# Optimization experiments

Measured on AMD Instinct MI355X. Metric: run time of the kernel, lower is better.

Reference implementation:

```python
import jax, jax.numpy as jnp
import numpy as np

NUM_HEADS = 16


def setup_inputs() -> dict:
    key = jax.random.key(0)
    ks = jax.random.split(key, 10)
    B, C, T, K, E = 2, 4, 512, 1024, 1024
    s = 0.02
    return {
        "hidden_states": jax.random.normal(ks[0], (B, T, E), jnp.float32),
        "key_value_states": jax.random.normal(ks[1], (B, C, K, E), jnp.float32),
        "Wq": jax.random.normal(ks[2], (E, E), jnp.float32) * s,
        "bq": jax.random.normal(ks[3], (E,), jnp.float32) * s,
        "Wk": jax.random.normal(ks[4], (E, E), jnp.float32) * s,
        "bk": jax.random.normal(ks[5], (E,), jnp.float32) * s,
        "Wv": jax.random.normal(ks[6], (E, E), jnp.float32) * s,
        "bv": jax.random.normal(ks[7], (E,), jnp.float32) * s,
        "Wo": jax.random.normal(ks[8], (E, E), jnp.float32) * s,
        "bo": jax.random.normal(ks[9], (E,), jnp.float32) * s,
    }


def reference(hidden_states, key_value_states, Wq, bq, Wk, bk, Wv, bv, Wo, bo):
    B, C, K, E = key_value_states.shape
    T = hidden_states.shape[1]
    H = NUM_HEADS
    Dh = E // H
    scaling = Dh ** (-0.5)
    # q: [B,H,T,Dh]
    q = ((hidden_states @ Wq.T + bq) * scaling).reshape(B, T, H, Dh).transpose(0, 2, 1, 3)
    # k, v: [B,H,K,C,Dh]  (matches torch view(B,C,K,H,Dh).transpose(1,3))
    k = (key_value_states @ Wk.T + bk).reshape(B, C, K, H, Dh).transpose(0, 3, 2, 1, 4)
    v = (key_value_states @ Wv.T + bv).reshape(B, C, K, H, Dh).transpose(0, 3, 2, 1, 4)
    # scores: [B,H,T,K,C]; softmax over kv_len axis (per channel)
    scores = jnp.einsum("bhtd,bhkcd->bhtkc", q, k)
    probs = jax.nn.softmax(scores, axis=3)
    # default channel pooling weight = 1/C (channel_weight=None path)
    cw = jnp.full((B, C), 1.0 / C, dtype=probs.dtype)
    # attend + weighted channel-sum -> [B,T,H,Dh] -> [B,T,E]
    attn = jnp.einsum("bhtkc,bhkcd,bc->bthd", probs, v, cw).reshape(B, T, E)
    return attn @ Wo.T + bo
```

## Files before the change

kernel.cpp:

```cpp
#include <hip/hip_runtime.h>
#include <hip/hip_bf16.h>

#define DIM_B 2
#define DIM_C 4
#define DIM_T 512
#define DIM_K 1024
#define DIM_E 1024
#define DIM_H 16
#define DIM_DH 64

typedef __attribute__((ext_vector_type(8))) short bf16x8;
typedef __attribute__((ext_vector_type(4))) short bf16x4;
typedef __attribute__((ext_vector_type(4))) float f32x4;
typedef __attribute__((ext_vector_type(2))) unsigned int u32x2;

#define MFMA_BF16(a, b, c) __builtin_amdgcn_mfma_f32_16x16x32_bf16((a), (b), (c), 0, 0, 0)

static __device__ __forceinline__ short f2bf(float f) {
    union { float f; unsigned u; } v; v.f = f;
    unsigned r = v.u + 0x7fffu + ((v.u >> 16) & 1u);
    return (short)(r >> 16);
}

static __device__ __forceinline__ unsigned pack_bf2(float lo, float hi) {
    union { float f; unsigned u; } a, b; a.f = lo; b.f = hi;
    return (a.u >> 16) | (b.u & 0xffff0000u);
}

static __device__ __forceinline__ void gload16(const short* g, short* lds) {
    __builtin_amdgcn_global_load_lds(
        (const __attribute__((address_space(1))) unsigned int*)g,
        (__attribute__((address_space(3))) unsigned int*)lds, 16, 0, 0);
}

__global__ __launch_bounds__(256) void cast6(
    const float* __restrict__ kvs, const float* __restrict__ hs,
    const float* __restrict__ wq, const float* __restrict__ wk,
    const float* __restrict__ wv, const float* __restrict__ wo,
    short* kvsb, short* hsb, short* wqb, short* wkb, short* wvb, short* wob)
{
    int blk = blockIdx.x;
    const float* src; short* dst; size_t off;
    if (blk < 4096) { src = kvs; dst = kvsb; off = (size_t)blk * 2048; }
    else {
        int s = (blk - 4096) >> 9;
        off = (size_t)((blk - 4096) & 511) * 2048;
        switch (s) {
            case 0: src = hs; dst = hsb; break;
            case 1: src = wq; dst = wqb; break;
            case 2: src = wk; dst = wkb; break;
            case 3: src = wv; dst = wvb; break;
            default: src = wo; dst = wob; break;
        }
    }
    size_t i = off + (size_t)threadIdx.x * 8;
    float4 a = *(const float4*)(src + i);
    float4 b = *(const float4*)(src + i + 4);
    bf16x8 o;
    o[0] = f2bf(a.x); o[1] = f2bf(a.y); o[2] = f2bf(a.z); o[3] = f2bf(a.w);
    o[4] = f2bf(b.x); o[5] = f2bf(b.y); o[6] = f2bf(b.z); o[7] = f2bf(b.w);
    *(bf16x8*)(dst + i) = o;
}

template <bool A_BF16, bool OUT_BF16, bool BIAS_ROW>
static __device__ __forceinline__ void gemm_tile(
    const void* __restrict__ Av, const short* __restrict__ W,
    const float* __restrict__ bias, void* __restrict__ Ov,
    int N, int Kd, float scale, int bm, int bn, short* As, short* Bs)
{
    const int tid = threadIdx.x;
    const int wave = tid >> 6, lane = tid & 63;
    const int L = lane & 15, Q = lane >> 4;
    const int wm = (wave & 1) * 64, wn = (wave >> 1) * 64;
    const int lr = lane >> 3;
    const int lc = ((lane & 7) ^ lr) * 8;

    f32x4 acc[4][4] = {};

    for (int k0 = 0; k0 < Kd; k0 += 64) {
        __syncthreads();
        if (A_BF16) {
            const short* A = (const short*)Av;
#pragma unroll
            for (int i = 0; i < 4; ++i) {
                int r = wave * 32 + i * 8;
                gload16(A + (size_t)(bm + r + lr) * Kd + k0 + lc, As + r * 64);
            }
        } else {
            const float* A = (const float*)Av;
#pragma unroll
            for (int rep = 0; rep < 4; ++rep) {
                int row = (tid >> 3) + rep * 32;
                int p = tid & 7;
                const float* src = A + (size_t)(bm + row) * Kd + k0 + p * 8;
                float4 a = *(const float4*)src;
                float4 b = *(const float4*)(src + 4);
                bf16x8 o;
                o[0] = f2bf(a.x); o[1] = f2bf(a.y); o[2] = f2bf(a.z); o[3] = f2bf(a.w);
                o[4] = f2bf(b.x); o[5] = f2bf(b.y); o[6] = f2bf(b.z); o[7] = f2bf(b.w);
                *(bf16x8*)&As[row * 64 + ((p ^ (row & 7)) * 8)] = o;
            }
        }
#pragma unroll
        for (int i = 0; i < 4; ++i) {
            int r = wave * 32 + i * 8;
            gload16(W + (size_t)(bn + r + lr) * Kd + k0 + lc, Bs + r * 64);
        }
        __syncthreads();
#pragma unroll
        for (int s = 0; s < 2; ++s) {
            bf16x8 af[4], bfr[4];
#pragma unroll
            for (int i = 0; i < 4; ++i)
                af[i] = *(const bf16x8*)&As[(wm + i * 16 + L) * 64 + (((s * 4 + Q) ^ (L & 7)) * 8)];
#pragma unroll
            for (int j = 0; j < 4; ++j)
                bfr[j] = *(const bf16x8*)&Bs[(wn + j * 16 + L) * 64 + (((s * 4 + Q) ^ (L & 7)) * 8)];
#pragma unroll
            for (int i = 0; i < 4; ++i)
#pragma unroll
                for (int j = 0; j < 4; ++j)
                    acc[i][j] = MFMA_BF16(af[i], bfr[j], acc[i][j]);
        }
    }

#pragma unroll
    for (int i = 0; i < 4; ++i) {
        int row0 = bm + wm + i * 16 + Q * 4;
#pragma unroll
        for (int j = 0; j < 4; ++j) {
            int col = bn + wn + j * 16 + L;
            float bj = BIAS_ROW ? 0.f : bias[col];
#pragma unroll
            for (int r = 0; r < 4; ++r) {
                float bb = BIAS_ROW ? bias[row0 + r] : bj;
                float o = (acc[i][j][r] + bb) * scale;
                if (OUT_BF16)
                    ((short*)Ov)[(size_t)(row0 + r) * N + col] = f2bf(o);
                else
                    ((float*)Ov)[(size_t)(row0 + r) * N + col] = o;
            }
        }
    }
}

template <bool A_BF16, bool OUT_BF16>
static __device__ __forceinline__ void gemm_tile64(
    const void* __restrict__ Av, const short* __restrict__ W,
    const float* __restrict__ bias, void* __restrict__ Ov,
    int N, int Kd, float scale, int bm, int bn, short* As, short* Bs)
{
    const int tid = threadIdx.x;
    const int wave = tid >> 6, lane = tid & 63;
    const int L = lane & 15, Q = lane >> 4;
    const int wm = (wave & 1) * 32, wn = (wave >> 1) * 32;
    const int lr = lane >> 3;
    const int lc = ((lane & 7) ^ lr) * 8;

    f32x4 acc[2][2] = {};

    for (int k0 = 0; k0 < Kd; k0 += 64) {
        __syncthreads();
        if (A_BF16) {
            const short* A = (const short*)Av;
#pragma unroll
            for (int i = 0; i < 2; ++i) {
                int r = wave * 16 + i * 8;
                gload16(A + (size_t)(bm + r + lr) * Kd + k0 + lc, As + r * 64);
            }
        } else {
            const float* A = (const float*)Av;
#pragma unroll
            for (int rep = 0; rep < 2; ++rep) {
                int row = (tid >> 3) + rep * 32;
                int p = tid & 7;
                const float* src = A + (size_t)(bm + row) * Kd + k0 + p * 8;
                float4 a = *(const float4*)src;
                float4 b = *(const float4*)(src + 4);
                bf16x8 o;
                o[0] = f2bf(a.x); o[1] = f2bf(a.y); o[2] = f2bf(a.z); o[3] = f2bf(a.w);
                o[4] = f2bf(b.x); o[5] = f2bf(b.y); o[6] = f2bf(b.z); o[7] = f2bf(b.w);
                *(bf16x8*)&As[row * 64 + ((p ^ (row & 7)) * 8)] = o;
            }
        }
#pragma unroll
        for (int i = 0; i < 2; ++i) {
            int r = wave * 16 + i * 8;
            gload16(W + (size_t)(bn + r + lr) * Kd + k0 + lc, Bs + r * 64);
        }
        __syncthreads();
#pragma unroll
        for (int s = 0; s < 2; ++s) {
            bf16x8 af[2], bfr[2];
#pragma unroll
            for (int i = 0; i < 2; ++i)
                af[i] = *(const bf16x8*)&As[(wm + i * 16 + L) * 64 + (((s * 4 + Q) ^ (L & 7)) * 8)];
#pragma unroll
            for (int j = 0; j < 2; ++j)
                bfr[j] = *(const bf16x8*)&Bs[(wn + j * 16 + L) * 64 + (((s * 4 + Q) ^ (L & 7)) * 8)];
#pragma unroll
            for (int i = 0; i < 2; ++i)
#pragma unroll
                for (int j = 0; j < 2; ++j)
                    acc[i][j] = MFMA_BF16(af[i], bfr[j], acc[i][j]);
        }
    }

#pragma unroll
    for (int i = 0; i < 2; ++i) {
        int row0 = bm + wm + i * 16 + Q * 4;
#pragma unroll
        for (int j = 0; j < 2; ++j) {
            int col = bn + wn + j * 16 + L;
            float bj = bias[col];
#pragma unroll
            for (int r = 0; r < 4; ++r) {
                float o = (acc[i][j][r] + bj) * scale;
                if (OUT_BF16)
                    ((short*)Ov)[(size_t)(row0 + r) * N + col] = f2bf(o);
                else
                    ((float*)Ov)[(size_t)(row0 + r) * N + col] = o;
            }
        }
    }
}

__global__ __launch_bounds__(256) void gemm_qkv(
    const short* __restrict__ hsb, const short* __restrict__ wqb,
    const float* __restrict__ bq, short* __restrict__ qb,
    const short* __restrict__ kvsb, const short* __restrict__ wkb,
    const float* __restrict__ bk, short* __restrict__ kb,
    const short* __restrict__ wvb, const float* __restrict__ bv,
    short* __restrict__ vtb)
{
    __shared__ alignas(16) short As[128 * 64];
    __shared__ alignas(16) short Bs[128 * 64];
    int blk = blockIdx.x;
    if (blk < 256) {
        int i = blk;
        int bm = (i & 7) + 8 * (i >> 7);
        int bn = (i >> 3) & 15;
        gemm_tile64<true, true>(hsb, wqb, bq, qb, DIM_E, DIM_E, 0.125f,
                                bm * 64, bn * 64, As, Bs);
    } else if (blk < 768) {
        int i = blk - 256;
        int bm = (i & 7) + 8 * (i >> 6);
        int bn = (i >> 3) & 7;
        gemm_tile<true, true, false>(kvsb, wkb, bk, kb, DIM_E, DIM_E, 1.0f,
                                     bm * 128, bn * 128, As, Bs);
    } else {
        int i = blk - 768;
        int bn = (i & 7) + 8 * (i >> 6);
        int bm = (i >> 3) & 7;
        gemm_tile<true, true, true>(wvb, kvsb, bv, vtb, DIM_B * DIM_C * DIM_K, DIM_E, 1.0f,
                                    bm * 128, bn * 128, As, Bs);
    }
}

__global__ __launch_bounds__(256) void gemm_o(
    const float* __restrict__ A, const short* __restrict__ W,
    const float* __restrict__ bias, float* __restrict__ Out)
{
    __shared__ alignas(16) short As[64 * 64];
    __shared__ alignas(16) short Bs[64 * 64];
    int i = blockIdx.x;
    int bm = (i & 7) + 8 * (i >> 7);
    int bn = (i >> 3) & 15;
    gemm_tile64<false, false>(A, W, bias, Out, DIM_E, DIM_E, 1.0f,
                              bm * 64, bn * 64, As, Bs);
}

__global__ __launch_bounds__(256) void attn_kernel(
    const short* __restrict__ q, const short* __restrict__ k,
    const short* __restrict__ vt, float* __restrict__ attn)
{
    __shared__ alignas(16) short Ks[64 * 64];
    __shared__ alignas(16) short Vs[64 * 64];
    __shared__ alignas(16) short Pl[4][16][72];

    const int tid = threadIdx.x;
    const int wave = tid >> 6, lane = tid & 63;
    const int L = lane & 15, Q = lane >> 4;
    const int lr = lane >> 3;
    const int lc = ((lane & 7) ^ lr) * 8;
    const int x = blockIdx.x;
    const int low = x & 7;
    const int c = low & 3, b = low >> 2;
    const int y = x >> 3;
    const int tt = y & 7, h = y >> 3;
    const int t0 = tt * 64;
    const int NKV = DIM_B * DIM_C * DIM_K;

    const size_t qrow = (size_t)(b * DIM_T + t0 + wave * 16 + L) * DIM_E + h * DIM_DH;
    const bf16x8 aq0 = *(const bf16x8*)(q + qrow + Q * 8);
    const bf16x8 aq1 = *(const bf16x8*)(q + qrow + 32 + Q * 8);

    const size_t kbase = (size_t)((b * DIM_C + c) * DIM_K) * DIM_E + h * DIM_DH;
    const size_t vbase = (size_t)(h * DIM_DH) * NKV + (b * DIM_C + c) * DIM_K;

    float lsum = 0.f;
    f32x4 oacc[4] = {};

    const int xs0 = (Q ^ (L & 7)) * 8;
    const int xs1 = ((4 + Q) ^ (L & 7)) * 8;

    for (int kc = 0; kc < 16; ++kc) {
        const int kk0 = kc * 64;
        __syncthreads();
#pragma unroll
        for (int i = 0; i < 2; ++i) {
            int r = wave * 16 + i * 8;
            gload16(k + kbase + (size_t)(kk0 + r + lr) * DIM_E + lc, Ks + r * 64);
        }
#pragma unroll
        for (int i = 0; i < 2; ++i) {
            int r = wave * 16 + i * 8;
            gload16(vt + vbase + (size_t)(r + lr) * NKV + kk0 + lc, Vs + r * 64);
        }
        __syncthreads();
        f32x4 s4[4];
#pragma unroll
        for (int j = 0; j < 4; ++j) {
            bf16x8 bk0 = *(const bf16x8*)&Ks[(j * 16 + L) * 64 + xs0];
            bf16x8 bk1 = *(const bf16x8*)&Ks[(j * 16 + L) * 64 + xs1];
            f32x4 z = {};
            z = MFMA_BF16(bk0, aq0, z);
            s4[j] = MFMA_BF16(bk1, aq1, z);
        }
#pragma unroll
        for (int j = 0; j < 4; ++j) {
            float p0 = __expf(s4[j][0]), p1 = __expf(s4[j][1]);
            float p2 = __expf(s4[j][2]), p3 = __expf(s4[j][3]);
            lsum += (p0 + p1) + (p2 + p3);
            u32x2 w;
            w[0] = pack_bf2(p0, p1);
            w[1] = pack_bf2(p2, p3);
            *(u32x2*)&Pl[wave][L][j * 16 + Q * 4] = w;
        }
        bf16x8 ap0 = *(const bf16x8*)&Pl[wave][L][Q * 8];
        bf16x8 ap1 = *(const bf16x8*)&Pl[wave][L][32 + Q * 8];
#pragma unroll
        for (int dt = 0; dt < 4; ++dt) {
            bf16x8 bv0 = *(const bf16x8*)&Vs[(dt * 16 + L) * 64 + xs0];
            bf16x8 bv1 = *(const bf16x8*)&Vs[(dt * 16 + L) * 64 + xs1];
            oacc[dt] = MFMA_BF16(ap0, bv0, oacc[dt]);
            oacc[dt] = MFMA_BF16(ap1, bv1, oacc[dt]);
        }
    }

    float lr_ = lsum;
    lr_ += __shfl_xor(lr_, 16);
    lr_ += __shfl_xor(lr_, 32);
    float linv[4];
#pragma unroll
    for (int r = 0; r < 4; ++r)
        linv[r] = 0.25f / __shfl(lr_, Q * 4 + r);

#pragma unroll
    for (int dt = 0; dt < 4; ++dt)
#pragma unroll
        for (int r = 0; r < 4; ++r) {
            int t = t0 + wave * 16 + Q * 4 + r;
            int d = dt * 16 + L;
            atomicAdd(&attn[(size_t)(b * DIM_T + t) * DIM_E + h * DIM_DH + d],
                      oacc[dt][r] * linv[r]);
        }
}

extern "C" void kernel_launch(void* const* d_in, const int* in_sizes, int n_in,
                              void* d_out, int out_size, void* d_ws, size_t ws_size,
                              hipStream_t stream)
{
    const float* hs  = (const float*)d_in[0];
    const float* kvs = (const float*)d_in[1];
    const float* Wq  = (const float*)d_in[2];
    const float* bq  = (const float*)d_in[3];
    const float* Wk  = (const float*)d_in[4];
    const float* bk  = (const float*)d_in[5];
    const float* Wv  = (const float*)d_in[6];
    const float* bv  = (const float*)d_in[7];
    const float* Wo  = (const float*)d_in[8];
    const float* bo  = (const float*)d_in[9];
    float* out = (float*)d_out;

    char* ws = (char*)d_ws;
    short* kvsb = (short*)(ws);
    short* hsb  = (short*)(ws + (16ull << 20));
    short* wqb  = (short*)(ws + (18ull << 20));
    short* wkb  = (short*)(ws + (20ull << 20));
    short* wvb  = (short*)(ws + (22ull << 20));
    short* wob  = (short*)(ws + (24ull << 20));
    short* qb   = (short*)(ws + (26ull << 20));
    short* kb   = (short*)(ws + (28ull << 20));
    short* vtb  = (short*)(ws + (44ull << 20));
    float* ab   = (float*)(ws + (16ull << 20));

    dim3 blk(256);
    const int MQ = DIM_B * DIM_T;

    cast6<<<dim3(4096 + 5 * 512), blk, 0, stream>>>(
        kvs, hs, Wq, Wk, Wv, Wo, kvsb, hsb, wqb, wkb, wvb, wob);

    gemm_qkv<<<dim3(256 + 512 + 512), blk, 0, stream>>>(
        hsb, wqb, bq, qb, kvsb, wkb, bk, kb, wvb, bv, vtb);

    (void)hipMemsetAsync(ab, 0, (size_t)MQ * DIM_E * sizeof(float), stream);

    attn_kernel<<<dim3(DIM_B * DIM_H * 8 * DIM_C), blk, 0, stream>>>(qb, kb, vtb, ab);

    gemm_o<<<dim3(256), blk, 0, stream>>>(ab, wob, bo, out);
}
```

Measured before the change: 211.1 us.

## Replace atomic attention accumulation with per-channel buffers summed in output GEMM

The attention kernel now writes each channel's partial result to its own fp32 buffer with plain stores instead of atomicAdd into one zeroed buffer. The output projection GEMM sums the four channel buffers while loading its A tile, which removes the memset and the atomic contention. The attention kernel also moves to 512-thread blocks covering 128 query rows, so each K/V tile is reused by twice as many waves. The cost is four times the intermediate write volume, which gemm_o must read back, and lower occupancy per block.

```diff
diff --git a/kernel.cpp b/kernel.cpp
--- a/kernel.cpp
+++ b/kernel.cpp
@@ -144,7 +144,7 @@
     }
 }
 
-template <bool A_BF16, bool OUT_BF16>
+template <bool A_BF16, bool OUT_BF16, int A_SUM>
 static __device__ __forceinline__ void gemm_tile64(
     const void* __restrict__ Av, const short* __restrict__ W,
     const float* __restrict__ bias, void* __restrict__ Ov,
@@ -174,12 +174,19 @@
             for (int rep = 0; rep < 2; ++rep) {
                 int row = (tid >> 3) + rep * 32;
                 int p = tid & 7;
-                const float* src = A + (size_t)(bm + row) * Kd + k0 + p * 8;
-                float4 a = *(const float4*)src;
-                float4 b = *(const float4*)(src + 4);
+                size_t base = (size_t)(bm + row) * Kd + k0 + p * 8;
+                float va[8] = {0.f, 0.f, 0.f, 0.f, 0.f, 0.f, 0.f, 0.f};
+#pragma unroll
+                for (int cc = 0; cc < A_SUM; ++cc) {
+                    const float* src = A + (size_t)cc * (1u << 20) + base;
+                    float4 a = *(const float4*)src;
+                    float4 b = *(const float4*)(src + 4);
+                    va[0] += a.x; va[1] += a.y; va[2] += a.z; va[3] += a.w;
+                    va[4] += b.x; va[5] += b.y; va[6] += b.z; va[7] += b.w;
+                }
                 bf16x8 o;
-                o[0] = f2bf(a.x); o[1] = f2bf(a.y); o[2] = f2bf(a.z); o[3] = f2bf(a.w);
-                o[4] = f2bf(b.x); o[5] = f2bf(b.y); o[6] = f2bf(b.z); o[7] = f2bf(b.w);
+#pragma unroll
+                for (int e = 0; e < 8; ++e) o[e] = f2bf(va[e]);
                 *(bf16x8*)&As[row * 64 + ((p ^ (row & 7)) * 8)] = o;
             }
         }
@@ -240,8 +247,8 @@
         int i = blk;
         int bm = (i & 7) + 8 * (i >> 7);
         int bn = (i >> 3) & 15;
-        gemm_tile64<true, true>(hsb, wqb, bq, qb, DIM_E, DIM_E, 0.125f,
-                                bm * 64, bn * 64, As, Bs);
+        gemm_tile64<true, true, 1>(hsb, wqb, bq, qb, DIM_E, DIM_E, 0.125f,
+                                   bm * 64, bn * 64, As, Bs);
     } else if (blk < 768) {
         int i = blk - 256;
         int bm = (i & 7) + 8 * (i >> 6);
@@ -266,17 +273,17 @@
     int i = blockIdx.x;
     int bm = (i & 7) + 8 * (i >> 7);
     int bn = (i >> 3) & 15;
-    gemm_tile64<false, false>(A, W, bias, Out, DIM_E, DIM_E, 1.0f,
-                              bm * 64, bn * 64, As, Bs);
-}
-
-__global__ __launch_bounds__(256) void attn_kernel(
+    gemm_tile64<false, false, 4>(A, W, bias, Out, DIM_E, DIM_E, 1.0f,
+                                 bm * 64, bn * 64, As, Bs);
+}
+
+__global__ __launch_bounds__(512) void attn_kernel(
     const short* __restrict__ q, const short* __restrict__ k,
-    const short* __restrict__ vt, float* __restrict__ attn)
+    const short* __restrict__ vt, float* __restrict__ abc)
 {
     __shared__ alignas(16) short Ks[64 * 64];
     __shared__ alignas(16) short Vs[64 * 64];
-    __shared__ alignas(16) short Pl[4][16][72];
+    __shared__ alignas(16) short Pl[8][16][72];
 
     const int tid = threadIdx.x;
     const int wave = tid >> 6, lane = tid & 63;
@@ -287,8 +294,8 @@
     const int low = x & 7;
     const int c = low & 3, b = low >> 2;
     const int y = x >> 3;
-    const int tt = y & 7, h = y >> 3;
-    const int t0 = tt * 64;
+    const int tt = y & 3, h = y >> 2;
+    const int t0 = tt * 128;
     const int NKV = DIM_B * DIM_C * DIM_K;
 
     const size_t qrow = (size_t)(b * DIM_T + t0 + wave * 16 + L) * DIM_E + h * DIM_DH;
@@ -307,14 +314,9 @@
     for (int kc = 0; kc < 16; ++kc) {
         const int kk0 = kc * 64;
         __syncthreads();
-#pragma unroll
-        for (int i = 0; i < 2; ++i) {
-            int r = wave * 16 + i * 8;
+        {
+            int r = wave * 8;
             gload16(k + kbase + (size_t)(kk0 + r + lr) * DIM_E + lc, Ks + r * 64);
-        }
-#pragma unroll
-        for (int i = 0; i < 2; ++i) {
-            int r = wave * 16 + i * 8;
             gload16(vt + vbase + (size_t)(r + lr) * NKV + kk0 + lc, Vs + r * 64);
         }
         __syncthreads();
@@ -356,14 +358,14 @@
     for (int r = 0; r < 4; ++r)
         linv[r] = 0.25f / __shfl(lr_, Q * 4 + r);
 
+    float* dst = abc + ((size_t)c << 20);
 #pragma unroll
     for (int dt = 0; dt < 4; ++dt)
 #pragma unroll
         for (int r = 0; r < 4; ++r) {
             int t = t0 + wave * 16 + Q * 4 + r;
             int d = dt * 16 + L;
-            atomicAdd(&attn[(size_t)(b * DIM_T + t) * DIM_E + h * DIM_DH + d],
-                      oacc[dt][r] * linv[r]);
+            dst[(size_t)(b * DIM_T + t) * DIM_E + h * DIM_DH + d] = oacc[dt][r] * linv[r];
         }
 }
 
@@ -393,10 +395,9 @@
     short* qb   = (short*)(ws + (26ull << 20));
     short* kb   = (short*)(ws + (28ull << 20));
     short* vtb  = (short*)(ws + (44ull << 20));
-    float* ab   = (float*)(ws + (16ull << 20));
+    float* abc  = (float*)(ws);
 
     dim3 blk(256);
-    const int MQ = DIM_B * DIM_T;
 
     cast6<<<dim3(4096 + 5 * 512), blk, 0, stream>>>(
         kvs, hs, Wq, Wk, Wv, Wo, kvsb, hsb, wqb, wkb, wvb, wob);
@@ -404,9 +405,7 @@
     gemm_qkv<<<dim3(256 + 512 + 512), blk, 0, stream>>>(
         hsb, wqb, bq, qb, kvsb, wkb, bk, kb, wvb, bv, vtb);
 
-    (void)hipMemsetAsync(ab, 0, (size_t)MQ * DIM_E * sizeof(float), stream);
-
-    attn_kernel<<<dim3(DIM_B * DIM_H * 8 * DIM_C), blk, 0, stream>>>(qb, kb, vtb, ab);
-
-    gemm_o<<<dim3(256), blk, 0, stream>>>(ab, wob, bo, out);
-}
+    attn_kernel<<<dim3(512), dim3(512), 0, stream>>>(qb, kb, vtb, abc);
+
+    gemm_o<<<dim3(256), blk, 0, stream>>>(abc, wob, bo, out);
+}
```

After: 211.3 us. About the same (+0.1%).
